# Optimization experiments

Measured on AMD Instinct MI355X. Metric: run time of the kernel, lower is better.

The kernel has to match this reference:

```python
import jax, jax.numpy as jnp
import numpy as np

D_BINS = 16   # piecewise-linear bins
N_PROP = 10   # hard-coded in CountModule.__init__


def pwl(w, x):
    """PiecewiseLinear.forward: w is [D_BINS+1], x any shape in [0,1]."""
    aw = jnp.abs(w)
    nw = aw / aw.sum()
    cs = jnp.cumsum(nw)               # [17] cumulative knot values
    xd = x * D_BINS
    ip = jnp.floor(xd).astype(jnp.int32)   # x >= 0 so trunc == floor
    frac = xd - ip.astype(x.dtype)
    return cs[jnp.minimum(ip, D_BINS)] + frac * nw[jnp.minimum(ip + 1, D_BINS)]


def iou(a):
    """Pairwise IoU of boxes a [B,4,n] (coords y1,x1,y2,x2) -> [B,n,n]."""
    tl = jnp.maximum(a[:, :2, :, None], a[:, :2, None, :])  # [B,2,n,n]
    br = jnp.minimum(a[:, 2:, :, None], a[:, 2:, None, :])
    wh = jnp.clip(br - tl, 0.0)
    inter = wh[:, 0] * wh[:, 1]                               # [B,n,n]
    area = jnp.clip(a[:, 2] - a[:, 0], 0.0) * jnp.clip(a[:, 3] - a[:, 1], 0.0)  # [B,n]
    return inter / (area[:, :, None] + area[:, None, :] - inter + 1e-12)


def count_forward(boxes, attention, f_weights):
    n = N_PROP
    B = boxes.shape[0]
    f = lambda i, x: pwl(f_weights[i], x)
    # keep top-n proposals by attention score
    att_v, idx = jax.lax.top_k(attention, n)                  # [B,n]
    boxes_f = jnp.take_along_axis(
        boxes, jnp.broadcast_to(idx[:, None, :], (B, 4, n)), axis=2)  # [B,4,n]
    att = jax.nn.sigmoid(att_v)
    A = att[:, :, None] * att[:, None, :]                     # outer product [B,n,n]
    Dm = 1.0 - iou(boxes_f)                                   # [B,n,n]
    A_t = f(0, A) * f(1, Dm)
    X = f(3, A) * f(4, Dm)
    # deduplicate: outer_diff on 2D att gives pairwise |a_i - a_j|; on 3D X the
    # original torch code unsqueezes both operands at the same axis, yielding zeros
    att_diff = jnp.abs(att[:, :, None] - att[:, None, :])     # [B,n,n]
    xs = X[:, :, None, :]
    score_diff = jnp.broadcast_to(jnp.abs(xs - xs), (B, n, n, n))  # zeros, as in torch
    sim = f(2, 1.0 - att_diff) * jnp.prod(f(2, 1.0 - score_diff), axis=1)  # [B,n,n]
    s_i = sim.sum(axis=2)                                     # [B,n]
    s_st = s_i[:, :, None] * s_i[:, None, :]                  # [B,n,n]
    score = A_t / s_st
    corr = f(0, att * att) / s_i
    mod_E = score.sum(axis=(1, 2))[:, None] + corr.sum(axis=1, keepdims=True)  # [B,1]
    c = jnp.sqrt(mod_E + 1e-20)
    # to_k_hot: soft two-hot over counts 0..n
    cc = jnp.clip(c, 0.0, float(n))                           # [B,1]
    ip = jnp.floor(cc).astype(jnp.int32)
    frac = cc - ip.astype(cc.dtype)
    left = jax.nn.one_hot(jnp.minimum(ip[:, 0], n), n + 1, dtype=cc.dtype)
    right = jax.nn.one_hot(jnp.minimum(ip[:, 0] + 1, n), n + 1, dtype=cc.dtype)
    o = (1.0 - frac) * left + frac * right                    # [B,n+1]
    p_a = jnp.abs(f(5, att) - 0.5)                            # [B,n]
    p_d = jnp.abs(f(6, Dm) - 0.5)                             # [B,n,n]
    gate = f(7, p_a.mean(axis=1, keepdims=True)
             + p_d.mean(axis=2).mean(axis=1, keepdims=True))  # [B,1]
    return gate * o                                           # [B,n+1]


def setup_inputs() -> dict:
    key = jax.random.key(0)
    k1, k2, k3 = jax.random.split(key, 3)
    B, M = 32768, 36
    boxes = jax.random.uniform(k1, (B, 4, M), dtype=jnp.float32)
    attention = jax.random.normal(k2, (B, M), dtype=jnp.float32)
    f_weights = jax.random.uniform(k3, (8, D_BINS + 1), dtype=jnp.float32,
                                   minval=0.25, maxval=1.75)
    return {"boxes": boxes, "attention": attention, "f_weights": f_weights}


def reference(boxes, attention, f_weights):
    return count_forward(boxes, attention, f_weights)
```

## Files before the change

kernel.cpp:

```cpp
#include <hip/hip_runtime.h>
#include <cstdint>
#include <cstddef>

#define MM 36
#define NP 10
#define BLOCK 256
#define GPB (BLOCK / 16)

template<int CTRL>
__device__ __forceinline__ float dpp_movf(float x) {
    return __int_as_float(__builtin_amdgcn_update_dpp(
        0, __float_as_int(x), CTRL, 0xF, 0xF, true));
}
__device__ __forceinline__ float rowmax16(float x) {
    x = fmaxf(x, dpp_movf<0xB1>(x));
    x = fmaxf(x, dpp_movf<0x4E>(x));
    x = fmaxf(x, dpp_movf<0x141>(x));
    x = fmaxf(x, dpp_movf<0x140>(x));
    return x;
}
__device__ __forceinline__ float rowsum16(float x) {
    x += dpp_movf<0xB1>(x);
    x += dpp_movf<0x4E>(x);
    x += dpp_movf<0x141>(x);
    x += dpp_movf<0x140>(x);
    return x;
}

__device__ __forceinline__ float pwl2(const float2* __restrict__ Trow, float x) {
    float xd = x * 16.0f;
    float fip = floorf(xd);
    float frac = xd - fip;
    int ip = (int)fminf(fip, 16.0f);
    float2 t = Trow[ip];
    return fmaf(frac, t.y, t.x);
}

__global__ __launch_bounds__(BLOCK) void count_kernel(
    const float* __restrict__ boxes,
    const float* __restrict__ attention,
    const float* __restrict__ fw,
    float* __restrict__ out,
    int B)
{
    __shared__ float2 T[8][17];
    __shared__ float4 T16[17];
    __shared__ float  boxrow[GPB][4 * MM];
    __shared__ float4 propA[GPB][NP];
    __shared__ float2 propB[GPB][NP];
    __shared__ __align__(8) float invl[GPB][NP];

    const int tid = threadIdx.x;
    const int lane = tid & 63;
    const int l    = tid & 15;
    const int g    = tid >> 4;
    int b = blockIdx.x * GPB + g;
    const bool valid = (b < B);
    b = valid ? b : (B - 1);

    const float* arow = attention + (size_t)b * MM;
    const float4* brow4 = reinterpret_cast<const float4*>(boxes + (size_t)b * (4 * MM));

    float v0 = arow[l];
    float v1 = arow[l + 16];
    float v2 = -INFINITY;
    if (l < 4) v2 = arow[l + 32];
    float4 B0 = brow4[l];
    float4 B1 = brow4[l + 16];
    float4 B2 = make_float4(0.f, 0.f, 0.f, 0.f);
    if (l < 4) B2 = brow4[l + 32];

    if (tid < 8) {
        const float* w = fw + tid * 17;
        float aw[17];
        float s = 0.f;
        #pragma unroll
        for (int k = 0; k < 17; ++k) { aw[k] = fabsf(w[k]); s += aw[k]; }
        float nw[17];
        #pragma unroll
        for (int k = 0; k < 17; ++k) nw[k] = aw[k] / s;
        float c = 0.f;
        #pragma unroll
        for (int k = 0; k < 17; ++k) {
            c += nw[k];
            T[tid][k] = make_float2(c, (k < 16) ? nw[k + 1] : nw[16]);
        }
    }
    if (tid < 17) {
        float2 a = T[1][tid];
        float2 c = T[6][tid];
        T16[tid] = make_float4(a.x, a.y, c.x, c.y);
    }

    float4* bls = reinterpret_cast<float4*>(&boxrow[g][0]);
    bls[l] = B0;
    bls[l + 16] = B1;
    if (l < 4) bls[l + 32] = B2;

    __syncthreads();

    const int gbase = tid & 48;
    int mi = 0; float mv = 0.f;
    #pragma unroll
    for (int t = 0; t < NP; ++t) {
        float vm = rowmax16(fmaxf(fmaxf(v0, v1), v2));
        unsigned long long b0 = __ballot(v0 == vm);
        unsigned long long b1 = __ballot(v1 == vm);
        unsigned long long b2 = __ballot(v2 == vm);
        unsigned g0 = (unsigned)(b0 >> gbase) & 0xFFFFu;
        unsigned g1 = (unsigned)(b1 >> gbase) & 0xFFFFu;
        unsigned g2 = (unsigned)(b2 >> gbase) & 0xFFFFu;
        int m = g0 ? (__ffs(g0) - 1)
              : (g1 ? (__ffs(g1) + 15)
                    : (__ffs(g2) + 31));
        if (l == t) { mi = m; mv = vm; }
        v0 = (m == l)      ? -INFINITY : v0;
        v1 = (m == l + 16) ? -INFINITY : v1;
        v2 = (m == l + 32) ? -INFINITY : v2;
    }

    float sattI = 0.f, y1I = 0.f, x1I = 0.f, y2I = 0.f, x2I = 0.f, areaI = 0.f;
    if (l < NP) {
        sattI = 1.0f / (1.0f + __expf(-mv));
        y1I = boxrow[g][mi];
        x1I = boxrow[g][mi + MM];
        y2I = boxrow[g][mi + 2 * MM];
        x2I = boxrow[g][mi + 3 * MM];
        areaI = fmaxf(y2I - y1I, 0.f) * fmaxf(x2I - x1I, 0.f);
        propA[g][l] = make_float4(y1I, x1I, y2I, x2I);
        propB[g][l] = make_float2(areaI, sattI);
    }

    float cs2_16 = T[2][16].x;
    float p2 = cs2_16 * cs2_16;
    float p4 = p2 * p2;
    float p8 = p4 * p4;
    float P = p8 * p2;

    const float2* T0 = &T[0][0];
    const float2* T2 = &T[2][0];
    const float2* T5 = &T[5][0];
    const float2* T7 = &T[7][0];

    float at[NP];
    float s_i = 0.f, pdAcc = 0.f;
    #pragma unroll
    for (int j = 0; j < NP; ++j) {
        float4 pj = propA[g][j];
        float2 qj = propB[g][j];
        float ty = fmaxf(y1I, pj.x);
        float tx = fmaxf(x1I, pj.y);
        float by = fminf(y2I, pj.z);
        float bx = fminf(x2I, pj.w);
        float inter = fmaxf(by - ty, 0.f) * fmaxf(bx - tx, 0.f);
        float iouv = __fdividef(inter, areaI + qj.x - inter + 1e-12f);
        float Dm = fmaxf(1.0f - iouv, 0.0f);
        float A = sattI * qj.y;
        float xdD = Dm * 16.0f;
        float fipD = floorf(xdD);
        float frD = xdD - fipD;
        int ipD = (int)fminf(fipD, 16.0f);
        float4 t16 = T16[ipD];
        float f1v = fmaf(frD, t16.y, t16.x);
        float f6v = fabsf(fmaf(frD, t16.w, t16.z) - 0.5f);
        at[j] = pwl2(T0, A) * f1v;
        s_i += pwl2(T2, 1.0f - fabsf(sattI - qj.y)) * P;
        pdAcc += f6v;
    }

    float inv_i = 1.0f / s_i;
    if (l < NP) invl[g][l] = inv_i;

    float dot = 0.f;
    const float2* ivp = reinterpret_cast<const float2*>(&invl[g][0]);
    #pragma unroll
    for (int jj = 0; jj < NP / 2; ++jj) {
        float2 iv = ivp[jj];
        dot = fmaf(at[2 * jj], iv.x, dot);
        dot = fmaf(at[2 * jj + 1], iv.y, dot);
    }

    float corr = pwl2(T0, sattI * sattI) * inv_i;
    float fmask = (l < NP) ? 1.f : 0.f;
    float contrib = fmask * (inv_i * dot + corr);
    float pav = fmask * fabsf(pwl2(T5, sattI) - 0.5f);
    float pdv = fmask * pdAcc;

    contrib = rowsum16(contrib);
    pav = rowsum16(pav);
    pdv = rowsum16(pdv);

    float gate = pwl2(T7, pav * 0.1f + pdv * 0.01f);
    float cval = sqrtf(contrib + 1e-20f);
    cval = fminf(fmaxf(cval, 0.f), 10.0f);
    float fip = floorf(cval);
    int ipc = (int)fip;
    float frac = cval - fip;
    int i0 = ipc < 10 ? ipc : 10;
    int i1 = (ipc + 1) < 10 ? (ipc + 1) : 10;

    if (valid && l < NP + 1) {
        float val = ((l == i0) ? (1.0f - frac) * gate : 0.f)
                  + ((l == i1) ? frac * gate : 0.f);
        out[(size_t)b * (NP + 1) + l] = val;
    }
}

extern "C" void kernel_launch(void* const* d_in, const int* in_sizes, int n_in,
                              void* d_out, int out_size, void* d_ws, size_t ws_size,
                              hipStream_t stream) {
    const float* boxes = (const float*)d_in[0];
    const float* attention = (const float*)d_in[1];
    const float* fw = (const float*)d_in[2];
    float* out = (float*)d_out;
    int B = in_sizes[1] / MM;
    int grid = (B + GPB - 1) / GPB;
    hipLaunchKernelGGL(count_kernel, dim3(grid), dim3(BLOCK), 0, stream,
                       boxes, attention, fw, out, B);
}
```

Before: 23.69 us.

## Precompute PWL tables in a separate kernel and read them from global memory

Moves the per-block normalization and cumsum of the eight piecewise-linear weight vectors into a tiny one-block kernel that writes packed tables to workspace. The main kernel then reads tables straight from global memory (cached), which removes the per-block table build, the LDS tables and the block-wide __syncthreads. Table lookups are clamped to 15 so 16-entry tables suffice. The cost is an extra kernel launch and global/L1 latency on the gathered table loads in place of LDS reads.

```diff
diff --git a/kernel.cpp b/kernel.cpp
--- a/kernel.cpp
+++ b/kernel.cpp
@@ -6,6 +6,7 @@
 #define NP 10
 #define BLOCK 256
 #define GPB (BLOCK / 16)
+
 
 template<int CTRL>
 __device__ __forceinline__ float dpp_movf(float x) {
@@ -27,33 +28,78 @@
     return x;
 }
 
-__device__ __forceinline__ float pwl2(const float2* __restrict__ Trow, float x) {
+__device__ __forceinline__ float pwl2g(const float2* __restrict__ T, float x) {
     float xd = x * 16.0f;
-    float fip = floorf(xd);
+    float fip = fminf(floorf(xd), 15.0f);
     float frac = xd - fip;
-    int ip = (int)fminf(fip, 16.0f);
-    float2 t = Trow[ip];
+    float2 t = T[(int)fip];
     return fmaf(frac, t.y, t.x);
+}
+
+__global__ __launch_bounds__(64) void table_kernel(
+    const float* __restrict__ fw, float* __restrict__ ws)
+{
+    const int f = threadIdx.x;
+    if (f >= 8) return;
+    const float* w = fw + f * 17;
+    float aw[17];
+    float s = 0.f;
+    #pragma unroll
+    for (int k = 0; k < 17; ++k) { aw[k] = fabsf(w[k]); s += aw[k]; }
+    float nw[17];
+    #pragma unroll
+    for (int k = 0; k < 17; ++k) nw[k] = aw[k] / s;
+    float cs[17];
+    float c = 0.f;
+    #pragma unroll
+    for (int k = 0; k < 17; ++k) { c += nw[k]; cs[k] = c; }
+
+    if (f == 1) {
+        #pragma unroll
+        for (int k = 0; k < 16; ++k) { ws[k * 4 + 0] = cs[k]; ws[k * 4 + 1] = nw[k + 1]; }
+    }
+    if (f == 6) {
+        #pragma unroll
+        for (int k = 0; k < 16; ++k) { ws[k * 4 + 2] = cs[k]; ws[k * 4 + 3] = nw[k + 1]; }
+    }
+    if (f == 0) {
+        #pragma unroll
+        for (int k = 0; k < 16; ++k) { ws[64 + 2 * k] = cs[k]; ws[65 + 2 * k] = nw[k + 1]; }
+    }
+    if (f == 2) {
+        #pragma unroll
+        for (int k = 0; k < 16; ++k) { ws[96 + 2 * k] = cs[k]; ws[97 + 2 * k] = nw[k + 1]; }
+        float cf = cs[16];
+        float p2 = cf * cf;
+        float p4 = p2 * p2;
+        float p8 = p4 * p4;
+        ws[192] = p8 * p2;
+    }
+    if (f == 5) {
+        #pragma unroll
+        for (int k = 0; k < 16; ++k) { ws[128 + 2 * k] = cs[k]; ws[129 + 2 * k] = nw[k + 1]; }
+    }
+    if (f == 7) {
+        #pragma unroll
+        for (int k = 0; k < 16; ++k) { ws[160 + 2 * k] = cs[k]; ws[161 + 2 * k] = nw[k + 1]; }
+    }
 }
 
 __global__ __launch_bounds__(BLOCK) void count_kernel(
     const float* __restrict__ boxes,
     const float* __restrict__ attention,
-    const float* __restrict__ fw,
+    const float* __restrict__ tabs,
     float* __restrict__ out,
     int B)
 {
-    __shared__ float2 T[8][17];
-    __shared__ float4 T16[17];
     __shared__ float  boxrow[GPB][4 * MM];
     __shared__ float4 propA[GPB][NP];
     __shared__ float2 propB[GPB][NP];
     __shared__ __align__(8) float invl[GPB][NP];
 
     const int tid = threadIdx.x;
-    const int lane = tid & 63;
-    const int l    = tid & 15;
-    const int g    = tid >> 4;
+    const int l   = tid & 15;
+    const int g   = tid >> 4;
     int b = blockIdx.x * GPB + g;
     const bool valid = (b < B);
     b = valid ? b : (B - 1);
@@ -70,34 +116,17 @@
     float4 B2 = make_float4(0.f, 0.f, 0.f, 0.f);
     if (l < 4) B2 = brow4[l + 32];
 
-    if (tid < 8) {
-        const float* w = fw + tid * 17;
-        float aw[17];
-        float s = 0.f;
-        #pragma unroll
-        for (int k = 0; k < 17; ++k) { aw[k] = fabsf(w[k]); s += aw[k]; }
-        float nw[17];
-        #pragma unroll
-        for (int k = 0; k < 17; ++k) nw[k] = aw[k] / s;
-        float c = 0.f;
-        #pragma unroll
-        for (int k = 0; k < 17; ++k) {
-            c += nw[k];
-            T[tid][k] = make_float2(c, (k < 16) ? nw[k + 1] : nw[16]);
-        }
-    }
-    if (tid < 17) {
-        float2 a = T[1][tid];
-        float2 c = T[6][tid];
-        T16[tid] = make_float4(a.x, a.y, c.x, c.y);
-    }
+    const float4* T16 = reinterpret_cast<const float4*>(tabs);
+    const float2* T0  = reinterpret_cast<const float2*>(tabs + 64);
+    const float2* T2  = reinterpret_cast<const float2*>(tabs + 96);
+    const float2* T5  = reinterpret_cast<const float2*>(tabs + 128);
+    const float2* T7  = reinterpret_cast<const float2*>(tabs + 160);
+    const float P = tabs[192];
 
     float4* bls = reinterpret_cast<float4*>(&boxrow[g][0]);
     bls[l] = B0;
     bls[l + 16] = B1;
     if (l < 4) bls[l + 32] = B2;
-
-    __syncthreads();
 
     const int gbase = tid & 48;
     int mi = 0; float mv = 0.f;
@@ -131,17 +160,6 @@
         propB[g][l] = make_float2(areaI, sattI);
     }
 
-    float cs2_16 = T[2][16].x;
-    float p2 = cs2_16 * cs2_16;
-    float p4 = p2 * p2;
-    float p8 = p4 * p4;
-    float P = p8 * p2;
-
-    const float2* T0 = &T[0][0];
-    const float2* T2 = &T[2][0];
-    const float2* T5 = &T[5][0];
-    const float2* T7 = &T[7][0];
-
     float at[NP];
     float s_i = 0.f, pdAcc = 0.f;
     #pragma unroll
@@ -157,14 +175,13 @@
         float Dm = fmaxf(1.0f - iouv, 0.0f);
         float A = sattI * qj.y;
         float xdD = Dm * 16.0f;
-        float fipD = floorf(xdD);
+        float fipD = fminf(floorf(xdD), 15.0f);
         float frD = xdD - fipD;
-        int ipD = (int)fminf(fipD, 16.0f);
-        float4 t16 = T16[ipD];
+        float4 t16 = T16[(int)fipD];
         float f1v = fmaf(frD, t16.y, t16.x);
         float f6v = fabsf(fmaf(frD, t16.w, t16.z) - 0.5f);
-        at[j] = pwl2(T0, A) * f1v;
-        s_i += pwl2(T2, 1.0f - fabsf(sattI - qj.y)) * P;
+        at[j] = pwl2g(T0, A) * f1v;
+        s_i += pwl2g(T2, 1.0f - fabsf(sattI - qj.y)) * P;
         pdAcc += f6v;
     }
 
@@ -180,17 +197,17 @@
         dot = fmaf(at[2 * jj + 1], iv.y, dot);
     }
 
-    float corr = pwl2(T0, sattI * sattI) * inv_i;
+    float corr = pwl2g(T0, sattI * sattI) * inv_i;
     float fmask = (l < NP) ? 1.f : 0.f;
     float contrib = fmask * (inv_i * dot + corr);
-    float pav = fmask * fabsf(pwl2(T5, sattI) - 0.5f);
+    float pav = fmask * fabsf(pwl2g(T5, sattI) - 0.5f);
     float pdv = fmask * pdAcc;
 
     contrib = rowsum16(contrib);
     pav = rowsum16(pav);
     pdv = rowsum16(pdv);
 
-    float gate = pwl2(T7, pav * 0.1f + pdv * 0.01f);
+    float gate = pwl2g(T7, pav * 0.1f + pdv * 0.01f);
     float cval = sqrtf(contrib + 1e-20f);
     cval = fminf(fmaxf(cval, 0.f), 10.0f);
     float fip = floorf(cval);
@@ -213,8 +230,10 @@
     const float* attention = (const float*)d_in[1];
     const float* fw = (const float*)d_in[2];
     float* out = (float*)d_out;
+    float* ws = (float*)d_ws;
     int B = in_sizes[1] / MM;
+    hipLaunchKernelGGL(table_kernel, dim3(1), dim3(64), 0, stream, fw, ws);
     int grid = (B + GPB - 1) / GPB;
     hipLaunchKernelGGL(count_kernel, dim3(grid), dim3(BLOCK), 0, stream,
-                       boxes, attention, fw, out, B);
-}
+                       boxes, attention, ws, out, B);
+}
```

After: 27.14 us. +14.6%, slower.

## Replicate PWL tables per wavefront and drop block-wide barrier

Applied to the files above, without the earlier changes.

Each wavefront now builds its own copy of the needed piecewise-linear tables (skipping unused tables 3 and 4) and writes the packed float4 table directly, which removes the __syncthreads between table construction, box staging and the top-k/IoU phase. This avoids the block-level barrier stall and lets the four waves run independently. Correctness then rests on intra-wavefront lockstep execution for the LDS writes and reads, with no explicit wave barrier, and each wave repeats the table setup work. The normalization division is also replaced by a reciprocal multiply.

```diff
diff --git a/kernel.cpp b/kernel.cpp
--- a/kernel.cpp
+++ b/kernel.cpp
@@ -6,6 +6,7 @@
 #define NP 10
 #define BLOCK 256
 #define GPB (BLOCK / 16)
+#define WPB (BLOCK / 64)
 
 template<int CTRL>
 __device__ __forceinline__ float dpp_movf(float x) {
@@ -27,12 +28,12 @@
     return x;
 }
 
-__device__ __forceinline__ float pwl2(const float2* __restrict__ Trow, float x) {
+__device__ __forceinline__ float pwl17(const float2* __restrict__ T, float x) {
     float xd = x * 16.0f;
     float fip = floorf(xd);
     float frac = xd - fip;
     int ip = (int)fminf(fip, 16.0f);
-    float2 t = Trow[ip];
+    float2 t = T[ip];
     return fmaf(frac, t.y, t.x);
 }
 
@@ -43,15 +44,16 @@
     float* __restrict__ out,
     int B)
 {
-    __shared__ float2 T[8][17];
-    __shared__ float4 T16[17];
+    __shared__ float2 Tw[WPB][4][17];
+    __shared__ float4 T16w[WPB][17];
     __shared__ float  boxrow[GPB][4 * MM];
     __shared__ float4 propA[GPB][NP];
     __shared__ float2 propB[GPB][NP];
     __shared__ __align__(8) float invl[GPB][NP];
 
-    const int tid = threadIdx.x;
+    const int tid  = threadIdx.x;
     const int lane = tid & 63;
+    const int w    = tid >> 6;
     const int l    = tid & 15;
     const int g    = tid >> 4;
     int b = blockIdx.x * GPB + g;
@@ -70,34 +72,40 @@
     float4 B2 = make_float4(0.f, 0.f, 0.f, 0.f);
     if (l < 4) B2 = brow4[l + 32];
 
-    if (tid < 8) {
-        const float* w = fw + tid * 17;
+    if (lane < 8 && lane != 3 && lane != 4) {
+        const float* wp = fw + lane * 17;
         float aw[17];
         float s = 0.f;
         #pragma unroll
-        for (int k = 0; k < 17; ++k) { aw[k] = fabsf(w[k]); s += aw[k]; }
+        for (int k = 0; k < 17; ++k) { aw[k] = fabsf(wp[k]); s += aw[k]; }
+        float is = __fdividef(1.0f, s);
         float nw[17];
         #pragma unroll
-        for (int k = 0; k < 17; ++k) nw[k] = aw[k] / s;
+        for (int k = 0; k < 17; ++k) nw[k] = aw[k] * is;
+        float cs[17];
         float c = 0.f;
         #pragma unroll
-        for (int k = 0; k < 17; ++k) {
-            c += nw[k];
-            T[tid][k] = make_float2(c, (k < 16) ? nw[k + 1] : nw[16]);
+        for (int k = 0; k < 17; ++k) { c += nw[k]; cs[k] = c; }
+
+        if (lane == 1 || lane == 6) {
+            float* dst = &T16w[w][0].x + ((lane == 1) ? 0 : 2);
+            #pragma unroll
+            for (int k = 0; k < 17; ++k) {
+                dst[4 * k]     = cs[k];
+                dst[4 * k + 1] = (k < 16) ? nw[k + 1] : nw[16];
+            }
+        } else {
+            int row = (lane == 0) ? 0 : (lane == 2) ? 1 : (lane == 5) ? 2 : 3;
+            #pragma unroll
+            for (int k = 0; k < 17; ++k)
+                Tw[w][row][k] = make_float2(cs[k], (k < 16) ? nw[k + 1] : nw[16]);
         }
-    }
-    if (tid < 17) {
-        float2 a = T[1][tid];
-        float2 c = T[6][tid];
-        T16[tid] = make_float4(a.x, a.y, c.x, c.y);
     }
 
     float4* bls = reinterpret_cast<float4*>(&boxrow[g][0]);
     bls[l] = B0;
     bls[l + 16] = B1;
     if (l < 4) bls[l + 32] = B2;
-
-    __syncthreads();
 
     const int gbase = tid & 48;
     int mi = 0; float mv = 0.f;
@@ -131,19 +139,20 @@
         propB[g][l] = make_float2(areaI, sattI);
     }
 
-    float cs2_16 = T[2][16].x;
-    float p2 = cs2_16 * cs2_16;
-    float p4 = p2 * p2;
-    float p8 = p4 * p4;
-    float P = p8 * p2;
-
-    const float2* T0 = &T[0][0];
-    const float2* T2 = &T[2][0];
-    const float2* T5 = &T[5][0];
-    const float2* T7 = &T[7][0];
+    const float2* T0 = &Tw[w][0][0];
+    const float2* T2 = &Tw[w][1][0];
+    const float2* T5 = &Tw[w][2][0];
+    const float2* T7 = &Tw[w][3][0];
+    const float4* T16 = &T16w[w][0];
+
+    float cs2_16 = T2[16].x;
+    float p2c = cs2_16 * cs2_16;
+    float p4c = p2c * p2c;
+    float p8c = p4c * p4c;
+    float P = p8c * p2c;
 
     float at[NP];
-    float s_i = 0.f, pdAcc = 0.f;
+    float s_um = 0.f, pdAcc = 0.f;
     #pragma unroll
     for (int j = 0; j < NP; ++j) {
         float4 pj = propA[g][j];
@@ -157,16 +166,16 @@
         float Dm = fmaxf(1.0f - iouv, 0.0f);
         float A = sattI * qj.y;
         float xdD = Dm * 16.0f;
-        float fipD = floorf(xdD);
+        float fipD = fminf(floorf(xdD), 16.0f);
         float frD = xdD - fipD;
-        int ipD = (int)fminf(fipD, 16.0f);
-        float4 t16 = T16[ipD];
+        float4 t16 = T16[(int)fipD];
         float f1v = fmaf(frD, t16.y, t16.x);
         float f6v = fabsf(fmaf(frD, t16.w, t16.z) - 0.5f);
-        at[j] = pwl2(T0, A) * f1v;
-        s_i += pwl2(T2, 1.0f - fabsf(sattI - qj.y)) * P;
+        at[j] = pwl17(T0, A) * f1v;
+        s_um += pwl17(T2, 1.0f - fabsf(sattI - qj.y));
         pdAcc += f6v;
     }
+    float s_i = s_um * P;
 
     float inv_i = 1.0f / s_i;
     if (l < NP) invl[g][l] = inv_i;
@@ -180,17 +189,17 @@
         dot = fmaf(at[2 * jj + 1], iv.y, dot);
     }
 
-    float corr = pwl2(T0, sattI * sattI) * inv_i;
+    float corr = pwl17(T0, sattI * sattI) * inv_i;
     float fmask = (l < NP) ? 1.f : 0.f;
     float contrib = fmask * (inv_i * dot + corr);
-    float pav = fmask * fabsf(pwl2(T5, sattI) - 0.5f);
+    float pav = fmask * fabsf(pwl17(T5, sattI) - 0.5f);
     float pdv = fmask * pdAcc;
 
     contrib = rowsum16(contrib);
     pav = rowsum16(pav);
     pdv = rowsum16(pdv);
 
-    float gate = pwl2(T7, pav * 0.1f + pdv * 0.01f);
+    float gate = pwl17(T7, pav * 0.1f + pdv * 0.01f);
     float cval = sqrtf(contrib + 1e-20f);
     cval = fminf(fmaxf(cval, 0.f), 10.0f);
     float fip = floorf(cval);
```

Result: no change. 23.85 us (+0.7%).
